# Optimization experiments

Hardware: AMD Instinct MI355X
Metric: run time of the kernel (lower is better)

## Reference

```python
import jax, jax.numpy as jnp
import numpy as np


def setup_inputs() -> dict:
    key = jax.random.key(0)
    k1, k2 = jax.random.split(key)
    B, S, N, M = 4, 4, 4096, 4096
    output_points = jax.random.normal(k1, (B, S, N, 3), dtype=jnp.float32)
    target_points = jax.random.normal(k2, (B, S, M, 3), dtype=jnp.float32)
    return {"output_points": output_points, "target_points": target_points, "n_samples": 4096}


def reference(output_points, target_points, n_samples):
    # output_points: [B,S,N,3], target_points: [B,S,M,3] (already sampled to n_samples pts)
    x2 = jnp.sum(output_points * output_points, axis=-1)  # [B,S,N]
    y2 = jnp.sum(target_points * target_points, axis=-1)  # [B,S,M]
    xy = jnp.einsum('bsnd,bsmd->bsnm', output_points, target_points)  # [B,S,N,M]
    # squared pairwise distances; clamp tiny negatives from fp error
    d2 = jnp.maximum(x2[..., :, None] + y2[..., None, :] - 2.0 * xy, 0.0)
    dist1 = jnp.min(d2, axis=-1)  # [B,S,N] NN dist output->target (squared)
    dist2 = jnp.min(d2, axis=-2)  # [B,S,M] NN dist target->output (squared)
    # dist_combined per (b,s) = mean(dist1) + mean(dist2); tensor is [S,B]
    chamfer = jnp.mean(dist1, axis=-1) + jnp.mean(dist2, axis=-1)  # [B,S]
    return chamfer.T  # [n_future_steps, batch_size]
```

## Files before the change

kernel.cpp:

```cpp
#include <hip/hip_runtime.h>


constexpr int B = 4, S = 4, NPTS = 4096, PAIRS = B * S;
constexpr int THREADS = 1024;
constexpr int WAVES = THREADS / 64;
constexpr int QPT = 8;
constexpr int QPB = 64 * QPT;
constexpr int QTILES = NPTS / QPB;
constexpr int SEG = NPTS / WAVES;

typedef float v2f __attribute__((ext_vector_type(2)));

#define PK_FMA_ZW(g, q, rzw)                                              \
  asm("v_pk_fma_f32 %0, %1, %2, %2 op_sel:[0,0,1] op_sel_hi:[1,0,1]"      \
      : "=v"(g) : "v"(q), "v"(rzw))
#define PK_FMA_Y(g, q, rxy)                                               \
  asm("v_pk_fma_f32 %0, %1, %2, %0 op_sel:[0,1,0] op_sel_hi:[1,1,1]"      \
      : "+v"(g) : "v"(q), "v"(rxy))
#define PK_FMA_X(g, q, rxy)                                               \
  asm("v_pk_fma_f32 %0, %1, %2, %0 op_sel:[0,0,0] op_sel_hi:[1,0,1]"      \
      : "+v"(g) : "v"(q), "v"(rxy))

__global__ __launch_bounds__(THREADS, 4)
void chamfer_pk3_kernel(const float* __restrict__ out_pts,
                        const float* __restrict__ tgt_pts,
                        float* __restrict__ out) {
  const int t     = threadIdx.x;
  const int l     = t & 63;
  const int wid   = t >> 6;
  const int qtile = blockIdx.x;
  const int pair  = blockIdx.y;
  const int dir   = blockIdx.z;

  const float* qbase = (dir == 0 ? out_pts : tgt_pts) + (size_t)pair * NPTS * 3;
  const float* rbase = (dir == 0 ? tgt_pts : out_pts) + (size_t)pair * NPTS * 3;

  __shared__ float4 sref[NPTS];

  #pragma unroll
  for (int k = 0; k < NPTS / THREADS; ++k) {
    const int i = t + k * THREADS;
    const float rx = rbase[3 * i], ry = rbase[3 * i + 1], rz = rbase[3 * i + 2];
    sref[i] = make_float4(rx, ry, rz, -0.5f * (rx * rx + ry * ry + rz * rz));
  }

  v2f qx[4], qy[4], qz[4];
  #pragma unroll
  for (int p = 0; p < 4; ++p) {
    const int q0 = qtile * QPB + (2 * p) * 64 + l;
    const int q1 = q0 + 64;
    qx[p] = v2f{qbase[3 * q0], qbase[3 * q1]};
    qy[p] = v2f{qbase[3 * q0 + 1], qbase[3 * q1 + 1]};
    qz[p] = v2f{qbase[3 * q0 + 2], qbase[3 * q1 + 2]};
  }

  float acc[QPT];
  #pragma unroll
  for (int j = 0; j < QPT; ++j) acc[j] = -3.0e38f;

  __syncthreads();

  const int base = wid * SEG;
  #pragma unroll 2
  for (int r = 0; r < SEG; r += 2) {
    const float4 rf0 = sref[base + r];
    const float4 rf1 = sref[base + r + 1];
    v2f rxy0; rxy0.x = rf0.x; rxy0.y = rf0.y;
    v2f rzw0; rzw0.x = rf0.z; rzw0.y = rf0.w;
    v2f rxy1; rxy1.x = rf1.x; rxy1.y = rf1.y;
    v2f rzw1; rzw1.x = rf1.z; rzw1.y = rf1.w;
    #pragma unroll
    for (int p = 0; p < 4; ++p) {
      v2f g0, g1;
      PK_FMA_ZW(g0, qz[p], rzw0);
      PK_FMA_Y (g0, qy[p], rxy0);
      PK_FMA_X (g0, qx[p], rxy0);
      PK_FMA_ZW(g1, qz[p], rzw1);
      PK_FMA_Y (g1, qy[p], rxy1);
      PK_FMA_X (g1, qx[p], rxy1);
      acc[2 * p]     = fmaxf(fmaxf(acc[2 * p], g0.x), g1.x);
      acc[2 * p + 1] = fmaxf(fmaxf(acc[2 * p + 1], g0.y), g1.y);
    }
  }

  __syncthreads();
  float* Sf = reinterpret_cast<float*>(sref);

  #pragma unroll
  for (int j = 0; j < QPT; ++j) Sf[wid * QPB + j * 64 + l] = acc[j];
  __syncthreads();

  if (t < QPB) {
    float g = Sf[t];
    #pragma unroll
    for (int w = 1; w < WAVES; ++w) g = fmaxf(g, Sf[w * QPB + t]);
    const int j = t >> 6, p = j >> 1, h = j & 1;
    const float x2 = qx[p][h] * qx[p][h] + qy[p][h] * qy[p][h] + qz[p][h] * qz[p][h];
    float d = fmaxf(fmaf(-2.0f, g, x2), 0.0f);
    #pragma unroll
    for (int off = 1; off < 64; off <<= 1) d += __shfl_xor(d, off, 64);
    if (l == 0) Sf[WAVES * QPB + (t >> 6)] = d;
  }
  __syncthreads();
  if (t == 0) {
    float ssum = 0.0f;
    #pragma unroll
    for (int w = 0; w < QPB / 64; ++w) ssum += Sf[WAVES * QPB + w];
    const int b = pair >> 2, s = pair & 3;
    atomicAdd(&out[s * B + b], ssum * (1.0f / NPTS));
  }
}

extern "C" void kernel_launch(void* const* d_in, const int* in_sizes, int n_in,
                              void* d_out, int out_size, void* d_ws, size_t ws_size,
                              hipStream_t stream) {
  const float* out_pts = (const float*)d_in[0];
  const float* tgt_pts = (const float*)d_in[1];
  float* out = (float*)d_out;

  hipMemsetAsync(out, 0, out_size * sizeof(float), stream);
  dim3 grid(QTILES, PAIRS, 2);
  chamfer_pk3_kernel<<<grid, THREADS, 0, stream>>>(out_pts, tgt_pts, out);
}
```

Before: 98.21 us.

## Compute chamfer distances with bf16 split-precision MFMA and column-partial reduction

Adds a pack kernel that turns each point into a 16-element bf16 vector (hi/lo splits of the coordinates and the norm term), so that one 32x32x16 bf16 MFMA yields the full -0.5*d2 tile at roughly fp32 accuracy. The main kernel computes each pair matrix only once and takes both row maxima and column maxima from it. Row maxima are reduced in place, while column maxima go to a workspace buffer that a third kernel reduces. This replaces the two-direction packed-FMA kernel with matrix-core work, at the cost of extra launches, workspace traffic and hi/lo split rounding error. The old kernel remains as a fallback when the workspace is too small.

New measurement: 130.2 us. +32.6%, slower.

```diff
diff --git a/kernel.cpp b/kernel.cpp
--- a/kernel.cpp
+++ b/kernel.cpp
@@ -1,16 +1,147 @@
 #include <hip/hip_runtime.h>
-
-
-constexpr int B = 4, S = 4, NPTS = 4096, PAIRS = B * S;
-constexpr int THREADS = 1024;
-constexpr int WAVES = THREADS / 64;
-constexpr int QPT = 8;
-constexpr int QPB = 64 * QPT;
-constexpr int QTILES = NPTS / QPB;
-constexpr int SEG = NPTS / WAVES;
+#include <hip/hip_bf16.h>
+
+
+constexpr int BB = 4, SS = 4, NPTS = 4096, PAIRS = 16;
+constexpr int BANDS = 32;
+constexpr int TPB = 256;
+
+typedef __bf16 bf16x8 __attribute__((ext_vector_type(8)));
+typedef float f32x16 __attribute__((ext_vector_type(16)));
+
+constexpr size_t APACK_BYTES = (size_t)PAIRS * NPTS * 16 * 2;
+constexpr size_t BPACK_OFF   = APACK_BYTES;
+constexpr size_t COLP_OFF    = 2 * APACK_BYTES;
+constexpr size_t COLP_BYTES  = (size_t)PAIRS * BANDS * NPTS * 4;
+constexpr size_t WS_NEED_MFMA = COLP_OFF + COLP_BYTES;
+
+__global__ void pack_kernel(const float* __restrict__ outp,
+                            const float* __restrict__ tgtp,
+                            __bf16* __restrict__ apack,
+                            __bf16* __restrict__ bpack) {
+  const int idx = blockIdx.x * TPB + threadIdx.x;
+  const int which = idx >> 16;
+  const int pn = idx & 65535;
+  const float* p = (which ? tgtp : outp) + (size_t)pn * 3;
+  const float x = p[0], y = p[1], z = p[2];
+  const float n2 = -0.5f * (x * x + y * y + z * z);
+  const __bf16 xh = (__bf16)x, yh = (__bf16)y, zh = (__bf16)z, nh = (__bf16)n2;
+  const __bf16 xl = (__bf16)(x - (float)xh);
+  const __bf16 yl = (__bf16)(y - (float)yh);
+  const __bf16 zl = (__bf16)(z - (float)zh);
+  const __bf16 nl = (__bf16)(n2 - (float)nh);
+  const __bf16 one = (__bf16)1.0f;
+  union { __bf16 h[16]; uint4 q[2]; } u;
+  if (which == 0) {
+    u.h[0]=xh; u.h[1]=xl; u.h[2]=xh; u.h[3]=xl;
+    u.h[4]=yh; u.h[5]=yl; u.h[6]=yh; u.h[7]=yl;
+    u.h[8]=zh; u.h[9]=zl; u.h[10]=zh; u.h[11]=zl;
+    u.h[12]=one; u.h[13]=one; u.h[14]=nh; u.h[15]=nl;
+    uint4* dst = (uint4*)(apack + (size_t)pn * 16);
+    dst[0] = u.q[0]; dst[1] = u.q[1];
+  } else {
+    u.h[0]=xh; u.h[1]=xh; u.h[2]=xl; u.h[3]=xl;
+    u.h[4]=yh; u.h[5]=yh; u.h[6]=yl; u.h[7]=yl;
+    u.h[8]=zh; u.h[9]=zh; u.h[10]=zl; u.h[11]=zl;
+    u.h[12]=nh; u.h[13]=nl; u.h[14]=one; u.h[15]=one;
+    uint4* dst = (uint4*)(bpack + (size_t)pn * 16);
+    dst[0] = u.q[0]; dst[1] = u.q[1];
+  }
+}
+
+__global__ __launch_bounds__(TPB, 2)
+void chamfer_mfma_kernel(const __bf16* __restrict__ apack,
+                         const __bf16* __restrict__ bpack,
+                         float* __restrict__ colp,
+                         float* __restrict__ out) {
+  const int t = threadIdx.x, l = t & 63, w = t >> 6;
+  const int band = blockIdx.x, pair = blockIdx.y;
+  const int c32 = l & 31, h = l >> 5;
+
+  __shared__ float cpart[4][1024];
+
+  const int row = band * 128 + w * 32 + c32;
+  const bf16x8 afrag =
+      *(const bf16x8*)(apack + ((size_t)pair * NPTS + row) * 16 + h * 8);
+
+  f32x16 zacc;
+  #pragma unroll
+  for (int i = 0; i < 16; ++i) zacc[i] = 0.0f;
+
+  float rowM[16];
+  #pragma unroll
+  for (int i = 0; i < 16; ++i) rowM[i] = -3.0e38f;
+
+  const __bf16* bbase = bpack + (size_t)pair * NPTS * 16;
+
+  for (int chunk = 0; chunk < 4; ++chunk) {
+    __syncthreads();
+    #pragma unroll 2
+    for (int ct = 0; ct < 32; ++ct) {
+      const int col = chunk * 1024 + ct * 32 + c32;
+      const bf16x8 bfrag = *(const bf16x8*)(bbase + (size_t)col * 16 + h * 8);
+      const f32x16 acc =
+          __builtin_amdgcn_mfma_f32_32x32x16_bf16(afrag, bfrag, zacc, 0, 0, 0);
+      #pragma unroll
+      for (int i = 0; i < 16; ++i) rowM[i] = fmaxf(rowM[i], acc[i]);
+      float m0 = fmaxf(acc[0], acc[1]),  m1 = fmaxf(acc[2], acc[3]);
+      float m2 = fmaxf(acc[4], acc[5]),  m3 = fmaxf(acc[6], acc[7]);
+      float m4 = fmaxf(acc[8], acc[9]),  m5 = fmaxf(acc[10], acc[11]);
+      float m6 = fmaxf(acc[12], acc[13]), m7 = fmaxf(acc[14], acc[15]);
+      float cm = fmaxf(fmaxf(fmaxf(m0, m1), fmaxf(m2, m3)),
+                       fmaxf(fmaxf(m4, m5), fmaxf(m6, m7)));
+      cm = fmaxf(cm, __shfl_xor(cm, 32, 64));
+      cpart[w][ct * 32 + c32] = cm;
+    }
+    __syncthreads();
+    const int c0 = t * 4;
+    float4 v;
+    v.x = fmaxf(fmaxf(cpart[0][c0+0], cpart[1][c0+0]), fmaxf(cpart[2][c0+0], cpart[3][c0+0]));
+    v.y = fmaxf(fmaxf(cpart[0][c0+1], cpart[1][c0+1]), fmaxf(cpart[2][c0+1], cpart[3][c0+1]));
+    v.z = fmaxf(fmaxf(cpart[0][c0+2], cpart[1][c0+2]), fmaxf(cpart[2][c0+2], cpart[3][c0+2]));
+    v.w = fmaxf(fmaxf(cpart[0][c0+3], cpart[1][c0+3]), fmaxf(cpart[2][c0+3], cpart[3][c0+3]));
+    *(float4*)(colp + ((size_t)(pair * BANDS + band)) * NPTS + chunk * 1024 + c0) = v;
+  }
+
+  #pragma unroll
+  for (int m = 1; m < 32; m <<= 1) {
+    #pragma unroll
+    for (int i = 0; i < 16; ++i)
+      rowM[i] = fmaxf(rowM[i], __shfl_xor(rowM[i], m, 64));
+  }
+  float s = 0.0f;
+  #pragma unroll
+  for (int i = 0; i < 16; ++i) s += fmaxf(-2.0f * rowM[i], 0.0f);
+  s += __shfl_xor(s, 32, 64);
+  if (l == 0) {
+    const int b = pair >> 2, sx = pair & 3;
+    atomicAdd(&out[sx * BB + b], s * (1.0f / NPTS));
+  }
+}
+
+__global__ void colred_kernel(const float* __restrict__ colp,
+                              float* __restrict__ out) {
+  const int t = threadIdx.x;
+  const int col = blockIdx.x * TPB + t;
+  const int pair = blockIdx.y;
+  const float* base = colp + (size_t)pair * BANDS * NPTS + col;
+  float g = -3.0e38f;
+  #pragma unroll 4
+  for (int bnd = 0; bnd < BANDS; ++bnd) g = fmaxf(g, base[(size_t)bnd * NPTS]);
+  float d = fmaxf(-2.0f * g, 0.0f);
+  #pragma unroll
+  for (int off = 1; off < 64; off <<= 1) d += __shfl_xor(d, off, 64);
+  __shared__ float red[4];
+  if ((t & 63) == 0) red[t >> 6] = d;
+  __syncthreads();
+  if (t == 0) {
+    const float ssum = red[0] + red[1] + red[2] + red[3];
+    const int b = pair >> 2, sx = pair & 3;
+    atomicAdd(&out[sx * BB + b], ssum * (1.0f / NPTS));
+  }
+}
 
 typedef float v2f __attribute__((ext_vector_type(2)));
-
 #define PK_FMA_ZW(g, q, rzw)                                              \
   asm("v_pk_fma_f32 %0, %1, %2, %2 op_sel:[0,0,1] op_sel_hi:[1,0,1]"      \
       : "=v"(g) : "v"(q), "v"(rzw))
@@ -21,93 +152,71 @@
   asm("v_pk_fma_f32 %0, %1, %2, %0 op_sel:[0,0,0] op_sel_hi:[1,0,1]"      \
       : "+v"(g) : "v"(q), "v"(rxy))
 
-__global__ __launch_bounds__(THREADS, 4)
+__global__ __launch_bounds__(1024, 4)
 void chamfer_pk3_kernel(const float* __restrict__ out_pts,
                         const float* __restrict__ tgt_pts,
                         float* __restrict__ out) {
-  const int t     = threadIdx.x;
-  const int l     = t & 63;
-  const int wid   = t >> 6;
-  const int qtile = blockIdx.x;
-  const int pair  = blockIdx.y;
-  const int dir   = blockIdx.z;
-
+  const int t = threadIdx.x, l = t & 63, wid = t >> 6;
+  const int qtile = blockIdx.x, pair = blockIdx.y, dir = blockIdx.z;
   const float* qbase = (dir == 0 ? out_pts : tgt_pts) + (size_t)pair * NPTS * 3;
   const float* rbase = (dir == 0 ? tgt_pts : out_pts) + (size_t)pair * NPTS * 3;
-
   __shared__ float4 sref[NPTS];
-
-  #pragma unroll
-  for (int k = 0; k < NPTS / THREADS; ++k) {
-    const int i = t + k * THREADS;
-    const float rx = rbase[3 * i], ry = rbase[3 * i + 1], rz = rbase[3 * i + 2];
-    sref[i] = make_float4(rx, ry, rz, -0.5f * (rx * rx + ry * ry + rz * rz));
-  }
-
+  #pragma unroll
+  for (int k = 0; k < 4; ++k) {
+    const int i = t + k * 1024;
+    const float rx = rbase[3*i], ry = rbase[3*i+1], rz = rbase[3*i+2];
+    sref[i] = make_float4(rx, ry, rz, -0.5f * (rx*rx + ry*ry + rz*rz));
+  }
   v2f qx[4], qy[4], qz[4];
   #pragma unroll
   for (int p = 0; p < 4; ++p) {
-    const int q0 = qtile * QPB + (2 * p) * 64 + l;
-    const int q1 = q0 + 64;
-    qx[p] = v2f{qbase[3 * q0], qbase[3 * q1]};
-    qy[p] = v2f{qbase[3 * q0 + 1], qbase[3 * q1 + 1]};
-    qz[p] = v2f{qbase[3 * q0 + 2], qbase[3 * q1 + 2]};
-  }
-
-  float acc[QPT];
-  #pragma unroll
-  for (int j = 0; j < QPT; ++j) acc[j] = -3.0e38f;
-
-  __syncthreads();
-
-  const int base = wid * SEG;
+    const int q0 = qtile * 512 + (2*p)*64 + l, q1 = q0 + 64;
+    qx[p] = v2f{qbase[3*q0],   qbase[3*q1]};
+    qy[p] = v2f{qbase[3*q0+1], qbase[3*q1+1]};
+    qz[p] = v2f{qbase[3*q0+2], qbase[3*q1+2]};
+  }
+  float acc[8];
+  #pragma unroll
+  for (int j = 0; j < 8; ++j) acc[j] = -3.0e38f;
+  __syncthreads();
+  const int base = wid * 256;
   #pragma unroll 2
-  for (int r = 0; r < SEG; r += 2) {
-    const float4 rf0 = sref[base + r];
-    const float4 rf1 = sref[base + r + 1];
-    v2f rxy0; rxy0.x = rf0.x; rxy0.y = rf0.y;
-    v2f rzw0; rzw0.x = rf0.z; rzw0.y = rf0.w;
-    v2f rxy1; rxy1.x = rf1.x; rxy1.y = rf1.y;
-    v2f rzw1; rzw1.x = rf1.z; rzw1.y = rf1.w;
+  for (int r = 0; r < 256; r += 2) {
+    const float4 rf0 = sref[base + r], rf1 = sref[base + r + 1];
+    v2f rxy0{rf0.x, rf0.y}, rzw0{rf0.z, rf0.w};
+    v2f rxy1{rf1.x, rf1.y}, rzw1{rf1.z, rf1.w};
     #pragma unroll
     for (int p = 0; p < 4; ++p) {
       v2f g0, g1;
-      PK_FMA_ZW(g0, qz[p], rzw0);
-      PK_FMA_Y (g0, qy[p], rxy0);
-      PK_FMA_X (g0, qx[p], rxy0);
-      PK_FMA_ZW(g1, qz[p], rzw1);
-      PK_FMA_Y (g1, qy[p], rxy1);
-      PK_FMA_X (g1, qx[p], rxy1);
-      acc[2 * p]     = fmaxf(fmaxf(acc[2 * p], g0.x), g1.x);
-      acc[2 * p + 1] = fmaxf(fmaxf(acc[2 * p + 1], g0.y), g1.y);
+      PK_FMA_ZW(g0, qz[p], rzw0); PK_FMA_Y(g0, qy[p], rxy0); PK_FMA_X(g0, qx[p], rxy0);
+      PK_FMA_ZW(g1, qz[p], rzw1); PK_FMA_Y(g1, qy[p], rxy1); PK_FMA_X(g1, qx[p], rxy1);
+      acc[2*p]   = fmaxf(fmaxf(acc[2*p],   g0.x), g1.x);
+      acc[2*p+1] = fmaxf(fmaxf(acc[2*p+1], g0.y), g1.y);
     }
   }
-
   __syncthreads();
   float* Sf = reinterpret_cast<float*>(sref);
-
-  #pragma unroll
-  for (int j = 0; j < QPT; ++j) Sf[wid * QPB + j * 64 + l] = acc[j];
-  __syncthreads();
-
-  if (t < QPB) {
+  #pragma unroll
+  for (int j = 0; j < 8; ++j) Sf[wid * 512 + j * 64 + l] = acc[j];
+  __syncthreads();
+  if (t < 512) {
     float g = Sf[t];
     #pragma unroll
-    for (int w = 1; w < WAVES; ++w) g = fmaxf(g, Sf[w * QPB + t]);
-    const int j = t >> 6, p = j >> 1, h = j & 1;
-    const float x2 = qx[p][h] * qx[p][h] + qy[p][h] * qy[p][h] + qz[p][h] * qz[p][h];
+    for (int w2 = 1; w2 < 16; ++w2) g = fmaxf(g, Sf[w2 * 512 + t]);
+    const int j = t >> 6, p = j >> 1, hh = j & 1;
+    const float x2 = qx[p][hh]*qx[p][hh] + qy[p][hh]*qy[p][hh] + qz[p][hh]*qz[p][hh];
     float d = fmaxf(fmaf(-2.0f, g, x2), 0.0f);
     #pragma unroll
     for (int off = 1; off < 64; off <<= 1) d += __shfl_xor(d, off, 64);
-    if (l == 0) Sf[WAVES * QPB + (t >> 6)] = d;
+    if (l == 0) Sf[16 * 512 + (t >> 6)] = d;
   }
   __syncthreads();
   if (t == 0) {
     float ssum = 0.0f;
     #pragma unroll
-    for (int w = 0; w < QPB / 64; ++w) ssum += Sf[WAVES * QPB + w];
-    const int b = pair >> 2, s = pair & 3;
-    atomicAdd(&out[s * B + b], ssum * (1.0f / NPTS));
+    for (int w2 = 0; w2 < 8; ++w2) ssum += Sf[16 * 512 + w2];
+    const int b = pair >> 2, sx = pair & 3;
+    atomicAdd(&out[sx * BB + b], ssum * (1.0f / NPTS));
   }
 }
 
@@ -119,6 +228,14 @@
   float* out = (float*)d_out;
 
   hipMemsetAsync(out, 0, out_size * sizeof(float), stream);
-  dim3 grid(QTILES, PAIRS, 2);
-  chamfer_pk3_kernel<<<grid, THREADS, 0, stream>>>(out_pts, tgt_pts, out);
-}
+  if (ws_size >= WS_NEED_MFMA) {
+    __bf16* apack = (__bf16*)((char*)d_ws);
+    __bf16* bpack = (__bf16*)((char*)d_ws + BPACK_OFF);
+    float*  colp  = (float*)((char*)d_ws + COLP_OFF);
+    pack_kernel<<<512, TPB, 0, stream>>>(out_pts, tgt_pts, apack, bpack);
+    chamfer_mfma_kernel<<<dim3(BANDS, PAIRS), TPB, 0, stream>>>(apack, bpack, colp, out);
+    colred_kernel<<<dim3(NPTS / TPB, PAIRS), TPB, 0, stream>>>(colp, out);
+  } else {
+    chamfer_pk3_kernel<<<dim3(8, PAIRS, 2), 1024, 0, stream>>>(out_pts, tgt_pts, out);
+  }
+}
```
